# Optimization experiments

Hardware: AMD Instinct MI355X
Metric: run time of the kernel (lower is better)

Reference implementation:

```python
import jax, jax.numpy as jnp
import numpy as np
from jax import lax

B, H, W, C = 4, 32, 32, 256
N_HEADS = 8
HEAD_D = C // N_HEADS  # 32


def position_encoding(height, width, channels):
    # Faithful to Position_Embedding: for size=256, dim=128; both even/odd use sin.
    dim = channels // 2
    y_embed = np.repeat(np.arange(1, height + 1), width).reshape(height, width)
    x_embed = np.broadcast_to(np.arange(1, width + 1), (height, width))
    div_term = 10000.0 ** (2 * (np.arange(dim) // 2) / dim)
    pos_x = x_embed[:, :, None] / div_term
    pos_y = y_embed[:, :, None] / div_term
    px = np.concatenate((np.sin(pos_x[:, :, 0::2]), np.sin(pos_x[:, :, 1::2])), axis=2)
    py = np.concatenate((np.sin(pos_y[:, :, 0::2]), np.sin(pos_y[:, :, 1::2])), axis=2)
    pe = np.concatenate((py, px), axis=2)[None].astype(np.float32)  # [1,H,W,C]
    return jnp.asarray(pe)


def setup_inputs() -> dict:
    key = jax.random.key(0)
    ks = jax.random.split(key, 10)
    s = 0.02  # weight init scale
    return {
        "src1": jax.random.normal(ks[0], (B, H, W, C), jnp.float32),
        "src2": jax.random.normal(ks[1], (B, H, W, C), jnp.float32),
        "Wq1": jax.random.normal(ks[2], (C, C), jnp.float32) * s,
        "bq1": jnp.zeros((C,), jnp.float32),
        "Wq2": jax.random.normal(ks[3], (C, C), jnp.float32) * s,
        "bq2": jnp.zeros((C,), jnp.float32),
        "Wk": jax.random.normal(ks[4], (C, C), jnp.float32) * s,
        "bk": jnp.zeros((C,), jnp.float32),
        "Wv": jax.random.normal(ks[5], (C, C), jnp.float32) * s,
        "bv": jnp.zeros((C,), jnp.float32),
        "conv_w": jax.random.normal(ks[6], (3, 3, 2 * HEAD_D, 2 * HEAD_D), jnp.float32) * s,
        "conv_b": jnp.zeros((2 * HEAD_D,), jnp.float32),
        "Wo": jax.random.normal(ks[7], (C, C), jnp.float32) * s,
        "bo": jnp.zeros((C,), jnp.float32),
    }


def reference(src1, src2, Wq1, bq1, Wq2, bq2, Wk, bk, Wv, bv, conv_w, conv_b, Wo, bo):
    d = HEAD_D
    N = H * W
    pe = position_encoding(H, W, C)  # [1,H,W,C]
    kin = src1 + pe
    q1_in = src1 + pe
    v_in = src1 + pe
    q2_in = src2 + pe

    q1 = q1_in @ Wq1 + bq1  # [B,H,W,C]
    q2 = q2_in @ Wq2 + bq2
    k = kin @ Wk + bk
    v = v_in @ Wv + bv

    # Q head split: 8 heads -> add first 4 and last 4 -> 4 effective heads
    Q1 = q1.reshape(B, N, 8, d)
    q_s_1 = Q1[:, :, :4, :] + Q1[:, :, 4:, :]  # [B,N,4,d]
    Q2 = q2.reshape(B, N, 8, d)
    q_s_2 = Q2[:, :, :4, :] + Q2[:, :, 4:, :]  # [B,N,4,d]

    # K split: self path (first 4d channels), co path (conv on 2d, concat last 2d)
    k_s = k[..., : 4 * d]  # [B,H,W,4d]
    k_co_1 = k[..., 4 * d : 6 * d]  # [B,H,W,2d]
    k_co_2 = k[..., 6 * d :]  # [B,H,W,2d]
    k_conv_r = lax.conv_general_dilated(
        k_co_1, conv_w, window_strides=(1, 1), padding="SAME",
        dimension_numbers=("NHWC", "HWIO", "NHWC")) + conv_b
    k_conv = jnp.concatenate([k_conv_r, k_co_2], axis=-1)  # [B,H,W,4d]

    k_s_1 = k_s.reshape(B, N, 4, d)
    k_s_2 = k_conv.reshape(B, N, 4, d)
    v_co = v.reshape(B, N, 8, d).transpose(0, 2, 1, 3)  # [B,8,N,d]

    scale = jnp.sqrt(jnp.float32(d))
    logits_self = jnp.einsum("bnhd,bmhd->bhnm", q_s_1, k_s_1) / scale  # [B,4,N,N]
    logits_co = jnp.einsum("bnhd,bmhd->bhnm", q_s_2, k_s_2) / scale  # [B,4,N,N]
    scaled = jnp.concatenate([logits_co, logits_self], axis=1)  # [B,8,N,N]

    attn = jax.nn.softmax(scaled, axis=-1)
    out = jnp.einsum("bhnm,bhmd->bnhd", attn, v_co).reshape(B, N, C)
    return out @ Wo + bo  # [B,N,C]
```

## Files before the change

kernel.cpp:

```cpp
#include <hip/hip_runtime.h>
#include <cstdint>
#include <cstddef>

typedef __attribute__((ext_vector_type(8))) short short8v;
typedef __attribute__((ext_vector_type(4))) short short4v;
typedef __attribute__((ext_vector_type(4))) float f32x4;
typedef unsigned short ushort_t;

__device__ inline unsigned short f2bf(float x) {
    unsigned int u = __float_as_uint(x);
    return (unsigned short)((u + 0x7FFFu + ((u >> 16) & 1u)) >> 16);
}

__global__ __launch_bounds__(256) void pe_prep_kernel(
    const float* __restrict__ src1, const float* __restrict__ src2,
    const float* __restrict__ Wq1, const float* __restrict__ Wq2,
    const float* __restrict__ Wk, const float* __restrict__ Wv,
    const float* __restrict__ Wo, const float* __restrict__ cw,
    const float* __restrict__ bq1, const float* __restrict__ bq2,
    const float* __restrict__ bk, const float* __restrict__ bv,
    ushort_t* __restrict__ X1, ushort_t* __restrict__ X2,
    ushort_t* __restrict__ WcatT, ushort_t* __restrict__ WoT,
    float* __restrict__ bcat, ushort_t* __restrict__ Wcv2)
{
    __shared__ ushort_t Ts[64][72];
    int bx = blockIdx.x;
    int t = threadIdx.x;

    if (bx < 1024) {
        int n = bx, c = t;
        int row = n >> 5, col = n & 31;
        float pos = (c < 128) ? (float)(row + 1) : (float)(col + 1);
        float freq = expf(-0.14391156831212787f * (float)(c & 63));
        float pe = sinf(pos * freq);
        for (int b = 0; b < 4; ++b) {
            size_t idx = ((size_t)b * 1024 + n) * 256 + c;
            X1[idx] = f2bf(src1[idx] + pe);
            X2[idx] = f2bf(src2[idx] + pe);
        }
        return;
    }

    if (bx < 1088) {
        int idx = bx - 1024;
        int kt = idx & 3, ct = idx >> 2;
        int k0 = kt * 64;
        const float* W; int csrc; int fold = 0; ushort_t* dst; int dstbase;
        if (ct < 2)       { W = Wq1; csrc = ct * 64;        fold = 1; dst = WcatT; dstbase = ct * 64; }
        else if (ct < 4)  { W = Wq2; csrc = (ct - 2) * 64;  fold = 1; dst = WcatT; dstbase = ct * 64; }
        else if (ct < 8)  { W = Wk;  csrc = (ct - 4) * 64;            dst = WcatT; dstbase = ct * 64; }
        else if (ct < 12) { W = Wv;  csrc = (ct - 8) * 64;            dst = WcatT; dstbase = ct * 64; }
        else              { W = Wo;  csrc = (ct - 12) * 64;           dst = WoT;   dstbase = (ct - 12) * 64; }
        if (kt == 0) {
            if (ct == 0 && t < 128) bcat[t] = bq1[t] + bq1[t + 128];
            if (ct == 2 && t < 128) bcat[128 + t] = bq2[t] + bq2[t + 128];
            if (ct == 4) bcat[256 + t] = bk[t];
            if (ct == 8) bcat[512 + t] = bv[t];
        }

        int kr = t >> 2, cq = t & 3;
        #pragma unroll
        for (int i = 0; i < 4; ++i) {
            int cc = cq * 16 + i * 4;
            float4 v = *(const float4*)&W[(size_t)(k0 + kr) * 256 + csrc + cc];
            if (fold) {
                float4 v2 = *(const float4*)&W[(size_t)(k0 + kr) * 256 + csrc + cc + 128];
                v.x += v2.x; v.y += v2.y; v.z += v2.z; v.w += v2.w;
            }
            Ts[kr][cc + 0] = f2bf(v.x); Ts[kr][cc + 1] = f2bf(v.y);
            Ts[kr][cc + 2] = f2bf(v.z); Ts[kr][cc + 3] = f2bf(v.w);
        }
        __syncthreads();
        int cr = t >> 2, kq = t & 3;
        ushort_t tmp[16];
        #pragma unroll
        for (int i = 0; i < 16; ++i) tmp[i] = Ts[kq * 16 + i][cr];
        *(short8v*)&dst[(size_t)(dstbase + cr) * 256 + k0 + kq * 16]     = *(short8v*)&tmp[0];
        *(short8v*)&dst[(size_t)(dstbase + cr) * 256 + k0 + kq * 16 + 8] = *(short8v*)&tmp[8];
        return;
    }

    {
        int tap = bx - 1088;
        int ci = t >> 2, co0 = (t & 3) * 16;
        #pragma unroll
        for (int i = 0; i < 16; ++i)
            Ts[ci][co0 + i] = f2bf(cw[((size_t)(tap * 64 + ci)) * 64 + co0 + i]);
        __syncthreads();
        int co = t >> 2, ci0 = (t & 3) * 16;
        ushort_t tmp[16];
        #pragma unroll
        for (int i = 0; i < 16; ++i) tmp[i] = Ts[ci0 + i][co];
        int kh = ci0 >> 5;
        int f = (tap * 2 + kh) * 4 + (co >> 4);
        int off = f * 512 + (co & 15) * 32 + (ci0 & 31);
        *(short8v*)&Wcv2[off]     = *(short8v*)&tmp[0];
        *(short8v*)&Wcv2[off + 8] = *(short8v*)&tmp[8];
    }
}

__global__ __launch_bounds__(256) void proj_gemm(
    const ushort_t* __restrict__ X1, const ushort_t* __restrict__ X2,
    const ushort_t* __restrict__ WcatT, const float* __restrict__ bcat,
    ushort_t* __restrict__ Qbf, ushort_t* __restrict__ Kbf,
    ushort_t* __restrict__ VTbf, ushort_t* __restrict__ CVbf)
{
    __shared__ ushort_t As[64][136];
    __shared__ ushort_t Bs[64][136];
    int colBase = blockIdx.x * 64, rowBase = blockIdx.y * 64;
    const ushort_t* A = (colBase >= 128 && colBase < 256) ? X2 : X1;
    int tid = threadIdx.x;
    int w = tid >> 6, l = tid & 63, lr = l & 15, g = l >> 4;
    int wr = w >> 1, wc = w & 1;
    int tr = tid >> 2, tq = tid & 3;
    f32x4 acc[2][2] = {};

    for (int kb = 0; kb < 256; kb += 128) {
        #pragma unroll
        for (int i = 0; i < 4; ++i)
            *(short8v*)&As[tr][tq * 32 + i * 8] =
                *(const short8v*)&A[(size_t)(rowBase + tr) * 256 + kb + tq * 32 + i * 8];
        #pragma unroll
        for (int i = 0; i < 4; ++i)
            *(short8v*)&Bs[tr][tq * 32 + i * 8] =
                *(const short8v*)&WcatT[(size_t)(colBase + tr) * 256 + kb + tq * 32 + i * 8];
        __syncthreads();
        #pragma unroll
        for (int ks = 0; ks < 4; ++ks) {
            short8v a0 = *(const short8v*)&As[wr * 32 + lr][ks * 32 + g * 8];
            short8v a1 = *(const short8v*)&As[wr * 32 + 16 + lr][ks * 32 + g * 8];
            short8v b0 = *(const short8v*)&Bs[wc * 32 + lr][ks * 32 + g * 8];
            short8v b1 = *(const short8v*)&Bs[wc * 32 + 16 + lr][ks * 32 + g * 8];
            acc[0][0] = __builtin_amdgcn_mfma_f32_16x16x32_bf16(a0, b0, acc[0][0], 0, 0, 0);
            acc[0][1] = __builtin_amdgcn_mfma_f32_16x16x32_bf16(a0, b1, acc[0][1], 0, 0, 0);
            acc[1][0] = __builtin_amdgcn_mfma_f32_16x16x32_bf16(a1, b0, acc[1][0], 0, 0, 0);
            acc[1][1] = __builtin_amdgcn_mfma_f32_16x16x32_bf16(a1, b1, acc[1][1], 0, 0, 0);
        }
        __syncthreads();
    }

    const float scale = 0.25503532182457352f;
    #pragma unroll
    for (int fr = 0; fr < 2; ++fr)
        #pragma unroll
        for (int fc = 0; fc < 2; ++fc) {
            int c = colBase + wc * 32 + fc * 16 + lr;
            float bv = bcat[c];
            int nb = rowBase + wr * 32 + fr * 16 + g * 4;
            int b = nb >> 10;
            if (c < 512) {
                #pragma unroll
                for (int r = 0; r < 4; ++r) {
                    int n = nb + r;
                    float v = acc[fr][fc][r] + bv;
                    if (c < 128) {
                        int h = 4 + (c >> 5), d = c & 31;
                        Qbf[(((size_t)(b * 8 + h) << 10) | (n & 1023)) * 32 + d] = f2bf(v * scale);
                    } else if (c < 256) {
                        int c2 = c - 128;
                        int h = c2 >> 5, d = c2 & 31;
                        Qbf[(((size_t)(b * 8 + h) << 10) | (n & 1023)) * 32 + d] = f2bf(v * scale);
                    } else {
                        int c3 = c - 256;
                        if (c3 < 128) {
                            int h = 4 + (c3 >> 5), d = c3 & 31;
                            Kbf[(((size_t)(b * 8 + h) << 10) | (n & 1023)) * 32 + d] = f2bf(v);
                        } else if (c3 < 192) {
                            CVbf[(size_t)n * 64 + (c3 - 128)] = f2bf(v);
                        } else {
                            int h = 2 + ((c3 - 192) >> 5), d = c3 & 31;
                            Kbf[(((size_t)(b * 8 + h) << 10) | (n & 1023)) * 32 + d] = f2bf(v);
                        }
                    }
                }
            } else {
                int c4 = c - 512;
                int h = c4 >> 5, d = c4 & 31;
                short4v pk;
                #pragma unroll
                for (int r = 0; r < 4; ++r) pk[r] = (short)f2bf(acc[fr][fc][r] + bv);
                *(short4v*)&VTbf[((size_t)((b * 8 + h) * 32 + d)) * 1024 + (nb & 1023)] = pk;
            }
        }
}

__global__ __launch_bounds__(256) void conv_mfma(
    const ushort_t* __restrict__ CVbf, const ushort_t* __restrict__ Wcv2,
    const float* __restrict__ cb, ushort_t* __restrict__ Kbf)
{
    __shared__ ushort_t Xs[8704];
    int blk = blockIdx.x;
    int b = blk >> 4, y0 = (blk & 15) * 2;
    int tid = threadIdx.x, w = tid >> 6, l = tid & 63, lr = l & 15, g = l >> 4;

    for (int p = tid >> 1; p < 136; p += 128) {
        int ry = p / 34, xc = p % 34;
        int ci0 = (tid & 1) * 32;
        int gy = y0 - 1 + ry, gx = xc - 1;
        int base = p << 6;
        int sw = (xc & 7) << 3;
        if ((unsigned)gy < 32u && (unsigned)gx < 32u) {
            const ushort_t* src = &CVbf[((size_t)(b * 1024 + gy * 32 + gx)) * 64 + ci0];
            #pragma unroll
            for (int k = 0; k < 4; ++k)
                *(short8v*)&Xs[(base + ci0 + k * 8) ^ sw] = *(const short8v*)&src[k * 8];
        } else {
            short8v z = {};
            #pragma unroll
            for (int k = 0; k < 4; ++k)
                *(short8v*)&Xs[(base + ci0 + k * 8) ^ sw] = z;
        }
    }
    __syncthreads();

    int yl = w >> 1, xb = (w & 1) * 16;
    f32x4 acc[4] = {};
    #pragma unroll
    for (int ky = 0; ky < 3; ++ky)
        #pragma unroll
        for (int kx = 0; kx < 3; ++kx) {
            int tap = ky * 3 + kx;
            #pragma unroll
            for (int kh = 0; kh < 2; ++kh) {
                int xa = xb + lr + kx;
                int e = (((yl + ky) * 34 + xa) << 6) + kh * 32 + g * 8;
                short8v af = *(const short8v*)&Xs[e ^ ((xa & 7) << 3)];
                int fb = (tap * 2 + kh) * 4 * 512 + lr * 32 + g * 8;
                #pragma unroll
                for (int nf = 0; nf < 4; ++nf) {
                    short8v bf_ = *(const short8v*)&Wcv2[fb + nf * 512];
                    acc[nf] = __builtin_amdgcn_mfma_f32_16x16x32_bf16(af, bf_, acc[nf], 0, 0, 0);
                }
            }
        }

    #pragma unroll
    for (int nf = 0; nf < 4; ++nf) {
        int co = nf * 16 + lr;
        float bias = cb[co];
        int h = co >> 5, d = co & 31;
        #pragma unroll
        for (int r = 0; r < 4; ++r) {
            int px = w * 16 + g * 4 + r;
            int n = y0 * 32 + px;
            Kbf[(((size_t)(b * 8 + h) << 10) | n) * 32 + d] = f2bf(acc[nf][r] + bias);
        }
    }
}

__global__ __launch_bounds__(256) void attn_mfma4(
    const ushort_t* __restrict__ Qbf, const ushort_t* __restrict__ Kbf,
    const ushort_t* __restrict__ VTbf, ushort_t* __restrict__ AObf)
{
    __shared__ ushort_t Kt[2][64][32];
    __shared__ ushort_t VT[2][32][72];
    __shared__ ushort_t Ps[4][16][72];

    int bh = blockIdx.y, q0 = blockIdx.x * 64;
    int tid = threadIdx.x, w = tid >> 6, l = tid & 63, lr = l & 15, g = l >> 4;
    int vd = tid >> 3, vn = (tid & 7) * 8;

    short8v qfrag = *(const short8v*)&Qbf[((size_t)bh * 1024 + q0 + w * 16 + lr) * 32 + g * 8];

    f32x4 accO[2] = {};
    float lsum = 0.f;
    const f32x4 zero = {};

    ((short8v*)&Kt[0][0][0])[tid] =
        *(const short8v*)&Kbf[((size_t)bh * 1024) * 32 + tid * 8];
    *(short8v*)&VT[0][vd][vn] =
        *(const short8v*)&VTbf[((size_t)bh * 32 + vd) * 1024 + vn];

    for (int mt = 0; mt < 16; ++mt) {
        int cur = mt & 1, nb = cur ^ 1;
        __syncthreads();

        short8v kreg, vreg;
        bool hasNext = (mt + 1) < 16;
        if (hasNext) {
            int m1 = (mt + 1) * 64;
            kreg = *(const short8v*)&Kbf[((size_t)bh * 1024 + m1) * 32 + tid * 8];
            vreg = *(const short8v*)&VTbf[((size_t)bh * 32 + vd) * 1024 + m1 + vn];
        }

        f32x4 st[4];
        #pragma unroll
        for (int t = 0; t < 4; ++t) {
            short8v kf = *(const short8v*)&Kt[cur][t * 16 + lr][g * 8];
            st[t] = __builtin_amdgcn_mfma_f32_16x16x32_bf16(kf, qfrag, zero, 0, 0, 0);
        }

        #pragma unroll
        for (int t = 0; t < 4; ++t) {
            float p0 = exp2f(st[t][0]), p1 = exp2f(st[t][1]);
            float p2 = exp2f(st[t][2]), p3 = exp2f(st[t][3]);
            lsum += (p0 + p1) + (p2 + p3);
            short4v pw;
            pw[0] = (short)f2bf(p0); pw[1] = (short)f2bf(p1);
            pw[2] = (short)f2bf(p2); pw[3] = (short)f2bf(p3);
            *(short4v*)&Ps[w][lr][t * 16 + g * 4] = pw;
        }

        #pragma unroll
        for (int kt = 0; kt < 2; ++kt) {
            short8v pa = *(const short8v*)&Ps[w][lr][kt * 32 + g * 8];
            #pragma unroll
            for (int nt = 0; nt < 2; ++nt) {
                short8v vb = *(const short8v*)&VT[cur][nt * 16 + lr][kt * 32 + g * 8];
                accO[nt] = __builtin_amdgcn_mfma_f32_16x16x32_bf16(pa, vb, accO[nt], 0, 0, 0);
            }
        }

        if (hasNext) {
            ((short8v*)&Kt[nb][0][0])[tid] = kreg;
            *(short8v*)&VT[nb][vd][vn] = vreg;
        }
    }

    lsum += __shfl_xor(lsum, 16);
    lsum += __shfl_xor(lsum, 32);

    int b = bh >> 3, h = bh & 7;
    #pragma unroll
    for (int r = 0; r < 4; ++r) {
        float lv = __uint_as_float((unsigned)__builtin_amdgcn_ds_bpermute(
            (g * 4 + r) * 4, (int)__float_as_uint(lsum)));
        float inv = 1.0f / lv;
        int n = q0 + w * 16 + g * 4 + r;
        #pragma unroll
        for (int nt = 0; nt < 2; ++nt)
            AObf[((size_t)(b * 1024 + n)) * 256 + h * 32 + nt * 16 + lr] =
                f2bf(accO[nt][r] * inv);
    }
}

__global__ __launch_bounds__(256) void out_gemm(
    const ushort_t* __restrict__ A, const ushort_t* __restrict__ WoT,
    const float* __restrict__ bo, float* __restrict__ out)
{
    __shared__ ushort_t As[64][136];
    __shared__ ushort_t Bs[64][136];
    int colBase = blockIdx.x * 64, rowBase = blockIdx.y * 64;
    int tid = threadIdx.x;
    int w = tid >> 6, l = tid & 63, lr = l & 15, g = l >> 4;
    int wr = w >> 1, wc = w & 1;
    int tr = tid >> 2, tq = tid & 3;
    f32x4 acc[2][2] = {};

    for (int kb = 0; kb < 256; kb += 128) {
        #pragma unroll
        for (int i = 0; i < 4; ++i)
            *(short8v*)&As[tr][tq * 32 + i * 8] =
                *(const short8v*)&A[(size_t)(rowBase + tr) * 256 + kb + tq * 32 + i * 8];
        #pragma unroll
        for (int i = 0; i < 4; ++i)
            *(short8v*)&Bs[tr][tq * 32 + i * 8] =
                *(const short8v*)&WoT[(size_t)(colBase + tr) * 256 + kb + tq * 32 + i * 8];
        __syncthreads();
        #pragma unroll
        for (int ks = 0; ks < 4; ++ks) {
            short8v a0 = *(const short8v*)&As[wr * 32 + lr][ks * 32 + g * 8];
            short8v a1 = *(const short8v*)&As[wr * 32 + 16 + lr][ks * 32 + g * 8];
            short8v b0 = *(const short8v*)&Bs[wc * 32 + lr][ks * 32 + g * 8];
            short8v b1 = *(const short8v*)&Bs[wc * 32 + 16 + lr][ks * 32 + g * 8];
            acc[0][0] = __builtin_amdgcn_mfma_f32_16x16x32_bf16(a0, b0, acc[0][0], 0, 0, 0);
            acc[0][1] = __builtin_amdgcn_mfma_f32_16x16x32_bf16(a0, b1, acc[0][1], 0, 0, 0);
            acc[1][0] = __builtin_amdgcn_mfma_f32_16x16x32_bf16(a1, b0, acc[1][0], 0, 0, 0);
            acc[1][1] = __builtin_amdgcn_mfma_f32_16x16x32_bf16(a1, b1, acc[1][1], 0, 0, 0);
        }
        __syncthreads();
    }

    #pragma unroll
    for (int fr = 0; fr < 2; ++fr)
        #pragma unroll
        for (int fc = 0; fc < 2; ++fc) {
            int c = colBase + wc * 32 + fc * 16 + lr;
            float bv = bo[c];
            int nb = rowBase + wr * 32 + fr * 16 + g * 4;
            #pragma unroll
            for (int r = 0; r < 4; ++r)
                out[(size_t)(nb + r) * 256 + c] = acc[fr][fc][r] + bv;
        }
}

extern "C" void kernel_launch(void* const* d_in, const int* in_sizes, int n_in,
                              void* d_out, int out_size, void* d_ws, size_t ws_size,
                              hipStream_t stream)
{
    const float* src1 = (const float*)d_in[0];
    const float* src2 = (const float*)d_in[1];
    const float* Wq1  = (const float*)d_in[2];
    const float* bq1  = (const float*)d_in[3];
    const float* Wq2  = (const float*)d_in[4];
    const float* bq2  = (const float*)d_in[5];
    const float* Wk   = (const float*)d_in[6];
    const float* bk   = (const float*)d_in[7];
    const float* Wv   = (const float*)d_in[8];
    const float* bv   = (const float*)d_in[9];
    const float* cw   = (const float*)d_in[10];
    const float* cb   = (const float*)d_in[11];
    const float* Wo   = (const float*)d_in[12];
    const float* bo   = (const float*)d_in[13];
    float* out = (float*)d_out;

    char* base = (char*)d_ws;
    const size_t MB = 1u << 20;
    const size_t KB = 1u << 10;
    ushort_t* X1bf = (ushort_t*)(base + 0 * MB);
    ushort_t* X2bf = (ushort_t*)(base + 2 * MB);
    ushort_t* Qbf  = (ushort_t*)(base + 4 * MB);
    ushort_t* Kbf  = (ushort_t*)(base + 6 * MB);
    ushort_t* VTbf = (ushort_t*)(base + 8 * MB);
    ushort_t* AObf = (ushort_t*)(base + 10 * MB);
    ushort_t* CVbf = (ushort_t*)(base + 12 * MB);
    ushort_t* WcatT= (ushort_t*)(base + 12 * MB + 512 * KB);
    ushort_t* WoT  = (ushort_t*)(base + 12 * MB + 896 * KB);
    float*    bcat = (float*)(base + 13 * MB);
    ushort_t* Wcv2 = (ushort_t*)(base + 13 * MB + 4 * KB);

    pe_prep_kernel<<<1097, 256, 0, stream>>>(
        src1, src2, Wq1, Wq2, Wk, Wv, Wo, cw, bq1, bq2, bk, bv,
        X1bf, X2bf, WcatT, WoT, bcat, Wcv2);
    proj_gemm<<<dim3(12, 64), 256, 0, stream>>>(
        X1bf, X2bf, WcatT, bcat, Qbf, Kbf, VTbf, CVbf);
    conv_mfma<<<64, 256, 0, stream>>>(CVbf, Wcv2, cb, Kbf);
    attn_mfma4<<<dim3(16, 32), 256, 0, stream>>>(Qbf, Kbf, VTbf, AObf);
    out_gemm<<<dim3(4, 64), 256, 0, stream>>>(AObf, WoT, bo, out);
}
```

Baseline: 48.69 us.

## Load MFMA operands directly from global memory, dropping LDS staging

The projection and output GEMMs no longer stage A and B tiles through shared memory. Each wave now loads its MFMA fragments straight from global memory in a fully unrolled K loop. The attention kernel likewise drops the double-buffered K/V shared tiles and their barriers, reading K and V^T fragments directly from global memory, which relies on L1/L2 for reuse across waves. This removes LDS traffic and __syncthreads, but adds redundant global loads, since waves sharing rows or columns fetch the same data, and exposes memory latency that is no longer hidden by prefetch.

After: 61.94 us. +27.2%, slower.

```diff
diff --git a/kernel.cpp b/kernel.cpp
--- a/kernel.cpp
+++ b/kernel.cpp
@@ -105,38 +105,29 @@
     ushort_t* __restrict__ Qbf, ushort_t* __restrict__ Kbf,
     ushort_t* __restrict__ VTbf, ushort_t* __restrict__ CVbf)
 {
-    __shared__ ushort_t As[64][136];
-    __shared__ ushort_t Bs[64][136];
     int colBase = blockIdx.x * 64, rowBase = blockIdx.y * 64;
     const ushort_t* A = (colBase >= 128 && colBase < 256) ? X2 : X1;
     int tid = threadIdx.x;
     int w = tid >> 6, l = tid & 63, lr = l & 15, g = l >> 4;
     int wr = w >> 1, wc = w & 1;
-    int tr = tid >> 2, tq = tid & 3;
     f32x4 acc[2][2] = {};
 
-    for (int kb = 0; kb < 256; kb += 128) {
-        #pragma unroll
-        for (int i = 0; i < 4; ++i)
-            *(short8v*)&As[tr][tq * 32 + i * 8] =
-                *(const short8v*)&A[(size_t)(rowBase + tr) * 256 + kb + tq * 32 + i * 8];
-        #pragma unroll
-        for (int i = 0; i < 4; ++i)
-            *(short8v*)&Bs[tr][tq * 32 + i * 8] =
-                *(const short8v*)&WcatT[(size_t)(colBase + tr) * 256 + kb + tq * 32 + i * 8];
-        __syncthreads();
-        #pragma unroll
-        for (int ks = 0; ks < 4; ++ks) {
-            short8v a0 = *(const short8v*)&As[wr * 32 + lr][ks * 32 + g * 8];
-            short8v a1 = *(const short8v*)&As[wr * 32 + 16 + lr][ks * 32 + g * 8];
-            short8v b0 = *(const short8v*)&Bs[wc * 32 + lr][ks * 32 + g * 8];
-            short8v b1 = *(const short8v*)&Bs[wc * 32 + 16 + lr][ks * 32 + g * 8];
-            acc[0][0] = __builtin_amdgcn_mfma_f32_16x16x32_bf16(a0, b0, acc[0][0], 0, 0, 0);
-            acc[0][1] = __builtin_amdgcn_mfma_f32_16x16x32_bf16(a0, b1, acc[0][1], 0, 0, 0);
-            acc[1][0] = __builtin_amdgcn_mfma_f32_16x16x32_bf16(a1, b0, acc[1][0], 0, 0, 0);
-            acc[1][1] = __builtin_amdgcn_mfma_f32_16x16x32_bf16(a1, b1, acc[1][1], 0, 0, 0);
-        }
-        __syncthreads();
+    const ushort_t* Ar0 = A + (size_t)(rowBase + wr * 32 + lr) * 256 + g * 8;
+    const ushort_t* Ar1 = Ar0 + 16 * 256;
+    const ushort_t* Br0 = WcatT + (size_t)(colBase + wc * 32 + lr) * 256 + g * 8;
+    const ushort_t* Br1 = Br0 + 16 * 256;
+
+    #pragma unroll
+    for (int k = 0; k < 8; ++k) {
+        int kk = k * 32;
+        short8v a0 = *(const short8v*)&Ar0[kk];
+        short8v a1 = *(const short8v*)&Ar1[kk];
+        short8v b0 = *(const short8v*)&Br0[kk];
+        short8v b1 = *(const short8v*)&Br1[kk];
+        acc[0][0] = __builtin_amdgcn_mfma_f32_16x16x32_bf16(a0, b0, acc[0][0], 0, 0, 0);
+        acc[0][1] = __builtin_amdgcn_mfma_f32_16x16x32_bf16(a0, b1, acc[0][1], 0, 0, 0);
+        acc[1][0] = __builtin_amdgcn_mfma_f32_16x16x32_bf16(a1, b0, acc[1][0], 0, 0, 0);
+        acc[1][1] = __builtin_amdgcn_mfma_f32_16x16x32_bf16(a1, b1, acc[1][1], 0, 0, 0);
     }
 
     const float scale = 0.25503532182457352f;
@@ -248,17 +239,17 @@
     }
 }
 
-__global__ __launch_bounds__(256) void attn_mfma4(
+__global__ __launch_bounds__(256) void attn_mfma5(
     const ushort_t* __restrict__ Qbf, const ushort_t* __restrict__ Kbf,
     const ushort_t* __restrict__ VTbf, ushort_t* __restrict__ AObf)
 {
-    __shared__ ushort_t Kt[2][64][32];
-    __shared__ ushort_t VT[2][32][72];
     __shared__ ushort_t Ps[4][16][72];
 
     int bh = blockIdx.y, q0 = blockIdx.x * 64;
     int tid = threadIdx.x, w = tid >> 6, l = tid & 63, lr = l & 15, g = l >> 4;
-    int vd = tid >> 3, vn = (tid & 7) * 8;
+
+    const ushort_t* Kbase = Kbf + (size_t)bh * 1024 * 32;
+    const ushort_t* Vbase = VTbf + (size_t)bh * 32 * 1024;
 
     short8v qfrag = *(const short8v*)&Qbf[((size_t)bh * 1024 + q0 + w * 16 + lr) * 32 + g * 8];
 
@@ -266,27 +257,13 @@
     float lsum = 0.f;
     const f32x4 zero = {};
 
-    ((short8v*)&Kt[0][0][0])[tid] =
-        *(const short8v*)&Kbf[((size_t)bh * 1024) * 32 + tid * 8];
-    *(short8v*)&VT[0][vd][vn] =
-        *(const short8v*)&VTbf[((size_t)bh * 32 + vd) * 1024 + vn];
-
     for (int mt = 0; mt < 16; ++mt) {
-        int cur = mt & 1, nb = cur ^ 1;
-        __syncthreads();
-
-        short8v kreg, vreg;
-        bool hasNext = (mt + 1) < 16;
-        if (hasNext) {
-            int m1 = (mt + 1) * 64;
-            kreg = *(const short8v*)&Kbf[((size_t)bh * 1024 + m1) * 32 + tid * 8];
-            vreg = *(const short8v*)&VTbf[((size_t)bh * 32 + vd) * 1024 + m1 + vn];
-        }
+        int m0 = mt * 64;
 
         f32x4 st[4];
         #pragma unroll
         for (int t = 0; t < 4; ++t) {
-            short8v kf = *(const short8v*)&Kt[cur][t * 16 + lr][g * 8];
+            short8v kf = *(const short8v*)&Kbase[(size_t)(m0 + t * 16 + lr) * 32 + g * 8];
             st[t] = __builtin_amdgcn_mfma_f32_16x16x32_bf16(kf, qfrag, zero, 0, 0, 0);
         }
 
@@ -306,14 +283,9 @@
             short8v pa = *(const short8v*)&Ps[w][lr][kt * 32 + g * 8];
             #pragma unroll
             for (int nt = 0; nt < 2; ++nt) {
-                short8v vb = *(const short8v*)&VT[cur][nt * 16 + lr][kt * 32 + g * 8];
+                short8v vb = *(const short8v*)&Vbase[(size_t)(nt * 16 + lr) * 1024 + m0 + kt * 32 + g * 8];
                 accO[nt] = __builtin_amdgcn_mfma_f32_16x16x32_bf16(pa, vb, accO[nt], 0, 0, 0);
             }
-        }
-
-        if (hasNext) {
-            ((short8v*)&Kt[nb][0][0])[tid] = kreg;
-            *(short8v*)&VT[nb][vd][vn] = vreg;
         }
     }
 
@@ -338,37 +310,28 @@
     const ushort_t* __restrict__ A, const ushort_t* __restrict__ WoT,
     const float* __restrict__ bo, float* __restrict__ out)
 {
-    __shared__ ushort_t As[64][136];
-    __shared__ ushort_t Bs[64][136];
     int colBase = blockIdx.x * 64, rowBase = blockIdx.y * 64;
     int tid = threadIdx.x;
     int w = tid >> 6, l = tid & 63, lr = l & 15, g = l >> 4;
     int wr = w >> 1, wc = w & 1;
-    int tr = tid >> 2, tq = tid & 3;
     f32x4 acc[2][2] = {};
 
-    for (int kb = 0; kb < 256; kb += 128) {
-        #pragma unroll
-        for (int i = 0; i < 4; ++i)
-            *(short8v*)&As[tr][tq * 32 + i * 8] =
-                *(const short8v*)&A[(size_t)(rowBase + tr) * 256 + kb + tq * 32 + i * 8];
-        #pragma unroll
-        for (int i = 0; i < 4; ++i)
-            *(short8v*)&Bs[tr][tq * 32 + i * 8] =
-                *(const short8v*)&WoT[(size_t)(colBase + tr) * 256 + kb + tq * 32 + i * 8];
-        __syncthreads();
-        #pragma unroll
-        for (int ks = 0; ks < 4; ++ks) {
-            short8v a0 = *(const short8v*)&As[wr * 32 + lr][ks * 32 + g * 8];
-            short8v a1 = *(const short8v*)&As[wr * 32 + 16 + lr][ks * 32 + g * 8];
-            short8v b0 = *(const short8v*)&Bs[wc * 32 + lr][ks * 32 + g * 8];
-            short8v b1 = *(const short8v*)&Bs[wc * 32 + 16 + lr][ks * 32 + g * 8];
-            acc[0][0] = __builtin_amdgcn_mfma_f32_16x16x32_bf16(a0, b0, acc[0][0], 0, 0, 0);
-            acc[0][1] = __builtin_amdgcn_mfma_f32_16x16x32_bf16(a0, b1, acc[0][1], 0, 0, 0);
-            acc[1][0] = __builtin_amdgcn_mfma_f32_16x16x32_bf16(a1, b0, acc[1][0], 0, 0, 0);
-            acc[1][1] = __builtin_amdgcn_mfma_f32_16x16x32_bf16(a1, b1, acc[1][1], 0, 0, 0);
-        }
-        __syncthreads();
+    const ushort_t* Ar0 = A + (size_t)(rowBase + wr * 32 + lr) * 256 + g * 8;
+    const ushort_t* Ar1 = Ar0 + 16 * 256;
+    const ushort_t* Br0 = WoT + (size_t)(colBase + wc * 32 + lr) * 256 + g * 8;
+    const ushort_t* Br1 = Br0 + 16 * 256;
+
+    #pragma unroll
+    for (int k = 0; k < 8; ++k) {
+        int kk = k * 32;
+        short8v a0 = *(const short8v*)&Ar0[kk];
+        short8v a1 = *(const short8v*)&Ar1[kk];
+        short8v b0 = *(const short8v*)&Br0[kk];
+        short8v b1 = *(const short8v*)&Br1[kk];
+        acc[0][0] = __builtin_amdgcn_mfma_f32_16x16x32_bf16(a0, b0, acc[0][0], 0, 0, 0);
+        acc[0][1] = __builtin_amdgcn_mfma_f32_16x16x32_bf16(a0, b1, acc[0][1], 0, 0, 0);
+        acc[1][0] = __builtin_amdgcn_mfma_f32_16x16x32_bf16(a1, b0, acc[1][0], 0, 0, 0);
+        acc[1][1] = __builtin_amdgcn_mfma_f32_16x16x32_bf16(a1, b1, acc[1][1], 0, 0, 0);
     }
 
     #pragma unroll
@@ -425,6 +388,6 @@
     proj_gemm<<<dim3(12, 64), 256, 0, stream>>>(
         X1bf, X2bf, WcatT, bcat, Qbf, Kbf, VTbf, CVbf);
     conv_mfma<<<64, 256, 0, stream>>>(CVbf, Wcv2, cb, Kbf);
-    attn_mfma4<<<dim3(16, 32), 256, 0, stream>>>(Qbf, Kbf, VTbf, AObf);
+    attn_mfma5<<<dim3(16, 32), 256, 0, stream>>>(Qbf, Kbf, VTbf, AObf);
     out_gemm<<<dim3(4, 64), 256, 0, stream>>>(AObf, WoT, bo, out);
 }
```

## Fold positional encoding into projection epilogue via precomputed PE·W tables

Applied to the files above, without the earlier changes.

Drops the separate pass that added the positional encoding to src1/src2 and wrote bf16 copies. Because the encoding splits into a row-only half and a column-only half, (x+pe)W becomes xW plus two small 32×768 tables (PE_y·W and PE_x·W). The prep kernel computes these tables with MFMA, and the projection GEMM now reads fp32 inputs directly, converts them to bf16 on load, and adds the table values in its epilogue. It also raises wave priority with s_setprio around the MFMA sections in attention. Each projection block now reads fp32 src twice as wide, and the table products are rounded in a different order than before.

Measured after the change: 57.14 us. +17.4%, slower.

```diff
diff --git a/kernel.cpp b/kernel.cpp
--- a/kernel.cpp
+++ b/kernel.cpp
@@ -12,38 +12,24 @@
     return (unsigned short)((u + 0x7FFFu + ((u >> 16) & 1u)) >> 16);
 }
 
-__global__ __launch_bounds__(256) void pe_prep_kernel(
-    const float* __restrict__ src1, const float* __restrict__ src2,
+__global__ __launch_bounds__(256) void prep_kernel(
     const float* __restrict__ Wq1, const float* __restrict__ Wq2,
     const float* __restrict__ Wk, const float* __restrict__ Wv,
     const float* __restrict__ Wo, const float* __restrict__ cw,
     const float* __restrict__ bq1, const float* __restrict__ bq2,
     const float* __restrict__ bk, const float* __restrict__ bv,
-    ushort_t* __restrict__ X1, ushort_t* __restrict__ X2,
     ushort_t* __restrict__ WcatT, ushort_t* __restrict__ WoT,
-    float* __restrict__ bcat, ushort_t* __restrict__ Wcv2)
+    float* __restrict__ bcat, ushort_t* __restrict__ Wcv2,
+    float* __restrict__ PEW)
 {
     __shared__ ushort_t Ts[64][72];
+    __shared__ ushort_t Tt[32][136];
+    __shared__ ushort_t Bs2[64][136];
     int bx = blockIdx.x;
     int t = threadIdx.x;
 
-    if (bx < 1024) {
-        int n = bx, c = t;
-        int row = n >> 5, col = n & 31;
-        float pos = (c < 128) ? (float)(row + 1) : (float)(col + 1);
-        float freq = expf(-0.14391156831212787f * (float)(c & 63));
-        float pe = sinf(pos * freq);
-        for (int b = 0; b < 4; ++b) {
-            size_t idx = ((size_t)b * 1024 + n) * 256 + c;
-            X1[idx] = f2bf(src1[idx] + pe);
-            X2[idx] = f2bf(src2[idx] + pe);
-        }
-        return;
-    }
-
-    if (bx < 1088) {
-        int idx = bx - 1024;
-        int kt = idx & 3, ct = idx >> 2;
+    if (bx < 64) {
+        int kt = bx & 3, ct = bx >> 2;
         int k0 = kt * 64;
         const float* W; int csrc; int fold = 0; ushort_t* dst; int dstbase;
         if (ct < 2)       { W = Wq1; csrc = ct * 64;        fold = 1; dst = WcatT; dstbase = ct * 64; }
@@ -57,7 +43,6 @@
             if (ct == 4) bcat[256 + t] = bk[t];
             if (ct == 8) bcat[512 + t] = bv[t];
         }
-
         int kr = t >> 2, cq = t & 3;
         #pragma unroll
         for (int i = 0; i < 4; ++i) {
@@ -80,8 +65,8 @@
         return;
     }
 
-    {
-        int tap = bx - 1088;
+    if (bx < 73) {
+        int tap = bx - 64;
         int ci = t >> 2, co0 = (t & 3) * 16;
         #pragma unroll
         for (int i = 0; i < 16; ++i)
@@ -96,19 +81,78 @@
         int off = f * 512 + (co & 15) * 32 + (ci0 & 31);
         *(short8v*)&Wcv2[off]     = *(short8v*)&tmp[0];
         *(short8v*)&Wcv2[off + 8] = *(short8v*)&tmp[8];
+        return;
+    }
+
+    {
+        int pidx = bx - 73;
+        int half = pidx / 12, ct2 = pidx % 12;
+        const float* W; int csrc; int fold = 0;
+        if (ct2 < 2)      { W = Wq1; csrc = ct2 * 64;       fold = 1; }
+        else if (ct2 < 4) { W = Wq2; csrc = (ct2 - 2) * 64; fold = 1; }
+        else if (ct2 < 8) { W = Wk;  csrc = (ct2 - 4) * 64; }
+        else              { W = Wv;  csrc = (ct2 - 8) * 64; }
+
+        #pragma unroll
+        for (int j = 0; j < 16; ++j) {
+            int idx2 = t * 16 + j;
+            int p = idx2 >> 7, k = idx2 & 127;
+            float freq = expf(-0.14391156831212787f * (float)(k & 63));
+            Tt[p][k] = f2bf(sinf((float)(p + 1) * freq));
+        }
+        #pragma unroll
+        for (int i = 0; i < 2; ++i) {
+            int k = (t >> 2) + i * 64;
+            int cbase = (t & 3) * 16;
+            #pragma unroll
+            for (int j2 = 0; j2 < 4; ++j2) {
+                float4 v = *(const float4*)&W[(size_t)(half * 128 + k) * 256 + csrc + cbase + j2 * 4];
+                if (fold) {
+                    float4 v2 = *(const float4*)&W[(size_t)(half * 128 + k) * 256 + csrc + cbase + j2 * 4 + 128];
+                    v.x += v2.x; v.y += v2.y; v.z += v2.z; v.w += v2.w;
+                }
+                Bs2[cbase + j2 * 4 + 0][k] = f2bf(v.x);
+                Bs2[cbase + j2 * 4 + 1][k] = f2bf(v.y);
+                Bs2[cbase + j2 * 4 + 2][k] = f2bf(v.z);
+                Bs2[cbase + j2 * 4 + 3][k] = f2bf(v.w);
+            }
+        }
+        __syncthreads();
+
+        int w = t >> 6, l = t & 63, lr = l & 15, g = l >> 4;
+        int mrow = w >> 1, cw2 = w & 1;
+        f32x4 acc2[2] = {};
+        #pragma unroll
+        for (int ks = 0; ks < 4; ++ks) {
+            short8v af = *(const short8v*)&Tt[mrow * 16 + lr][ks * 32 + g * 8];
+            #pragma unroll
+            for (int fc = 0; fc < 2; ++fc) {
+                short8v bf_ = *(const short8v*)&Bs2[cw2 * 32 + fc * 16 + lr][ks * 32 + g * 8];
+                acc2[fc] = __builtin_amdgcn_mfma_f32_16x16x32_bf16(af, bf_, acc2[fc], 0, 0, 0);
+            }
+        }
+        #pragma unroll
+        for (int fc = 0; fc < 2; ++fc)
+            #pragma unroll
+            for (int r = 0; r < 4; ++r) {
+                int p = mrow * 16 + g * 4 + r;
+                int c = ct2 * 64 + cw2 * 32 + fc * 16 + lr;
+                PEW[half * 24576 + p * 768 + c] = acc2[fc][r];
+            }
     }
 }
 
 __global__ __launch_bounds__(256) void proj_gemm(
-    const ushort_t* __restrict__ X1, const ushort_t* __restrict__ X2,
+    const float* __restrict__ src1, const float* __restrict__ src2,
     const ushort_t* __restrict__ WcatT, const float* __restrict__ bcat,
+    const float* __restrict__ PEW,
     ushort_t* __restrict__ Qbf, ushort_t* __restrict__ Kbf,
     ushort_t* __restrict__ VTbf, ushort_t* __restrict__ CVbf)
 {
     __shared__ ushort_t As[64][136];
     __shared__ ushort_t Bs[64][136];
     int colBase = blockIdx.x * 64, rowBase = blockIdx.y * 64;
-    const ushort_t* A = (colBase >= 128 && colBase < 256) ? X2 : X1;
+    const float* A = (colBase >= 128 && colBase < 256) ? src2 : src1;
     int tid = threadIdx.x;
     int w = tid >> 6, l = tid & 63, lr = l & 15, g = l >> 4;
     int wr = w >> 1, wc = w & 1;
@@ -117,9 +161,14 @@
 
     for (int kb = 0; kb < 256; kb += 128) {
         #pragma unroll
-        for (int i = 0; i < 4; ++i)
-            *(short8v*)&As[tr][tq * 32 + i * 8] =
-                *(const short8v*)&A[(size_t)(rowBase + tr) * 256 + kb + tq * 32 + i * 8];
+        for (int i = 0; i < 4; ++i) {
+            const float* ap = &A[(size_t)(rowBase + tr) * 256 + kb + tq * 32 + i * 8];
+            float4 v0 = *(const float4*)ap;
+            float4 v1 = *(const float4*)(ap + 4);
+            ushort_t tmp8[8] = {f2bf(v0.x), f2bf(v0.y), f2bf(v0.z), f2bf(v0.w),
+                                f2bf(v1.x), f2bf(v1.y), f2bf(v1.z), f2bf(v1.w)};
+            *(short8v*)&As[tr][tq * 32 + i * 8] = *(short8v*)tmp8;
+        }
         #pragma unroll
         for (int i = 0; i < 4; ++i)
             *(short8v*)&Bs[tr][tq * 32 + i * 8] =
@@ -148,11 +197,14 @@
             float bv = bcat[c];
             int nb = rowBase + wr * 32 + fr * 16 + g * 4;
             int b = nb >> 10;
+            int nn = nb & 1023;
+            float pey = PEW[(nn >> 5) * 768 + c];
             if (c < 512) {
                 #pragma unroll
                 for (int r = 0; r < 4; ++r) {
                     int n = nb + r;
-                    float v = acc[fr][fc][r] + bv;
+                    float pex = PEW[24576 + ((nn & 31) + r) * 768 + c];
+                    float v = acc[fr][fc][r] + bv + pey + pex;
                     if (c < 128) {
                         int h = 4 + (c >> 5), d = c & 31;
                         Qbf[(((size_t)(b * 8 + h) << 10) | (n & 1023)) * 32 + d] = f2bf(v * scale);
@@ -178,7 +230,10 @@
                 int h = c4 >> 5, d = c4 & 31;
                 short4v pk;
                 #pragma unroll
-                for (int r = 0; r < 4; ++r) pk[r] = (short)f2bf(acc[fr][fc][r] + bv);
+                for (int r = 0; r < 4; ++r) {
+                    float pex = PEW[24576 + ((nn & 31) + r) * 768 + c];
+                    pk[r] = (short)f2bf(acc[fr][fc][r] + bv + pey + pex);
+                }
                 *(short4v*)&VTbf[((size_t)((b * 8 + h) * 32 + d)) * 1024 + (nb & 1023)] = pk;
             }
         }
@@ -284,11 +339,13 @@
         }
 
         f32x4 st[4];
+        __builtin_amdgcn_s_setprio(1);
         #pragma unroll
         for (int t = 0; t < 4; ++t) {
             short8v kf = *(const short8v*)&Kt[cur][t * 16 + lr][g * 8];
             st[t] = __builtin_amdgcn_mfma_f32_16x16x32_bf16(kf, qfrag, zero, 0, 0, 0);
         }
+        __builtin_amdgcn_s_setprio(0);
 
         #pragma unroll
         for (int t = 0; t < 4; ++t) {
@@ -301,6 +358,7 @@
             *(short4v*)&Ps[w][lr][t * 16 + g * 4] = pw;
         }
 
+        __builtin_amdgcn_s_setprio(1);
         #pragma unroll
         for (int kt = 0; kt < 2; ++kt) {
             short8v pa = *(const short8v*)&Ps[w][lr][kt * 32 + g * 8];
@@ -310,6 +368,7 @@
                 accO[nt] = __builtin_amdgcn_mfma_f32_16x16x32_bf16(pa, vb, accO[nt], 0, 0, 0);
             }
         }
+        __builtin_amdgcn_s_setprio(0);
 
         if (hasNext) {
             ((short8v*)&Kt[nb][0][0])[tid] = kreg;
@@ -407,23 +466,22 @@
     char* base = (char*)d_ws;
     const size_t MB = 1u << 20;
     const size_t KB = 1u << 10;
-    ushort_t* X1bf = (ushort_t*)(base + 0 * MB);
-    ushort_t* X2bf = (ushort_t*)(base + 2 * MB);
-    ushort_t* Qbf  = (ushort_t*)(base + 4 * MB);
-    ushort_t* Kbf  = (ushort_t*)(base + 6 * MB);
-    ushort_t* VTbf = (ushort_t*)(base + 8 * MB);
-    ushort_t* AObf = (ushort_t*)(base + 10 * MB);
-    ushort_t* CVbf = (ushort_t*)(base + 12 * MB);
-    ushort_t* WcatT= (ushort_t*)(base + 12 * MB + 512 * KB);
-    ushort_t* WoT  = (ushort_t*)(base + 12 * MB + 896 * KB);
-    float*    bcat = (float*)(base + 13 * MB);
-    ushort_t* Wcv2 = (ushort_t*)(base + 13 * MB + 4 * KB);
-
-    pe_prep_kernel<<<1097, 256, 0, stream>>>(
-        src1, src2, Wq1, Wq2, Wk, Wv, Wo, cw, bq1, bq2, bk, bv,
-        X1bf, X2bf, WcatT, WoT, bcat, Wcv2);
+    ushort_t* Qbf  = (ushort_t*)(base + 0 * MB);
+    ushort_t* Kbf  = (ushort_t*)(base + 2 * MB);
+    ushort_t* VTbf = (ushort_t*)(base + 4 * MB);
+    ushort_t* AObf = (ushort_t*)(base + 6 * MB);
+    ushort_t* CVbf = (ushort_t*)(base + 8 * MB);
+    ushort_t* WcatT= (ushort_t*)(base + 8 * MB + 512 * KB);
+    ushort_t* WoT  = (ushort_t*)(base + 8 * MB + 896 * KB);
+    float*    bcat = (float*)(base + 9 * MB);
+    ushort_t* Wcv2 = (ushort_t*)(base + 9 * MB + 4 * KB);
+    float*    PEW  = (float*)(base + 9 * MB + 128 * KB);
+
+    prep_kernel<<<97, 256, 0, stream>>>(
+        Wq1, Wq2, Wk, Wv, Wo, cw, bq1, bq2, bk, bv,
+        WcatT, WoT, bcat, Wcv2, PEW);
     proj_gemm<<<dim3(12, 64), 256, 0, stream>>>(
-        X1bf, X2bf, WcatT, bcat, Qbf, Kbf, VTbf, CVbf);
+        src1, src2, WcatT, bcat, PEW, Qbf, Kbf, VTbf, CVbf);
     conv_mfma<<<64, 256, 0, stream>>>(CVbf, Wcv2, cb, Kbf);
     attn_mfma4<<<dim3(16, 32), 256, 0, stream>>>(Qbf, Kbf, VTbf, AObf);
     out_gemm<<<dim3(4, 64), 256, 0, stream>>>(AObf, WoT, bo, out);
```
